# Optimization experiments

Measured on AMD Instinct MI355X. Metric: run time of the kernel, lower is better.

## Reference

```python
import jax, jax.numpy as jnp
import numpy as np

NUM_COND = 16  # num_conditions
EPS = 1e-5


def setup_inputs() -> dict:
    key = jax.random.key(0)
    k1, k2, k3, k4 = jax.random.split(key, 4)
    N, F = 500000, 128
    x = jax.random.normal(k1, (N, F), dtype=jnp.float32)
    labels = jax.random.randint(k2, (N,), 0, NUM_COND)
    gamma = jax.random.uniform(k3, (NUM_COND, F), dtype=jnp.float32)
    beta = jax.random.normal(k4, (NUM_COND, F), dtype=jnp.float32)
    return {"x": x, "labels": labels, "gamma": gamma, "beta": beta}


def reference(x, labels, gamma, beta):
    # Conditional BatchNorm1d (training mode): per-label batch statistics
    # over the samples of each group, then per-label affine transform.
    num_cond = gamma.shape[0]
    ones = jnp.ones((x.shape[0],), x.dtype)
    counts = jax.ops.segment_sum(ones, labels, num_segments=num_cond)   # [C]
    counts = jnp.maximum(counts, 1.0)                                    # guard empty groups
    s1 = jax.ops.segment_sum(x, labels, num_segments=num_cond)          # [C,F]
    s2 = jax.ops.segment_sum(x * x, labels, num_segments=num_cond)      # [C,F]
    mean = s1 / counts[:, None]
    var = s2 / counts[:, None] - mean * mean                             # biased var (BatchNorm)
    inv_std = jax.lax.rsqrt(var + EPS)                                   # [C,F]
    scale = gamma * inv_std                                              # [C,F]
    shift = beta - mean * scale                                          # [C,F]
    y = x * scale[labels] + shift[labels]                                # fused gather + affine
    return y
```

## Files before the change

kernel.cpp:

```cpp
#include <hip/hip_runtime.h>

#define NUM_COND 16
#define FDIM 128
#define EPS 1e-5f
#define WPB 2
#define NSLOT 3
#define PB 4160
#define NCHUNK 16
#define MAXNB 1024

typedef float __attribute__((ext_vector_type(4))) f4v;
__device__ __forceinline__ void nt_store4(float4* p, const float4& v) {
    f4v t = { v.x, v.y, v.z, v.w };
    __builtin_nontemporal_store(t, (f4v*)p);
}

__global__ __launch_bounds__(128) void cbn_stats_kernel(
    const float* __restrict__ x, const int* __restrict__ labels,
    float* __restrict__ ws, int N, int Npairs, int pchunk)
{
    __shared__ float acc[WPB][4096];
    __shared__ float stage[WPB][NSLOT * 256];
    const int t = threadIdx.x;
    const int w = t >> 6;
    const int lane = t & 63;
    const int half = lane >> 5;
    const int sl = lane & 31;

    {
        float4* z = (float4*)acc[w];
        for (int i = lane; i < 1024; i += 64) z[i] = make_float4(0.f, 0.f, 0.f, 0.f);
    }

    const int pbeg = blockIdx.x * pchunk;
    const int pend = min(Npairs, pbeg + pchunk);
    const float4* x4 = (const float4*)x;
    float2* r1 = (float2*)acc[w];
    float2* r2 = r1 + 1024;
    float4* stg4 = (float4*)stage[w];
    float2* stg2 = (float2*)stage[w];

    int cnt = 0;
    float4 v0, v1, v2;
    int la0 = 0, la1 = 0, la2 = 0, lb0 = 0, lb1 = 0, lb2 = 0;
    v0 = v1 = v2 = make_float4(0.f, 0.f, 0.f, 0.f);

#define LOADSLOT(S, P)                                                  \
    {   const int p_ = (P);                                             \
        if (p_ < pend) {                                                \
            const int r_ = min(2 * p_ + half, N - 1);                   \
            v##S = x4[(size_t)r_ * 32 + sl];                            \
            la##S = labels[2 * p_];                                     \
            lb##S = labels[min(2 * p_ + 1, N - 1)];                     \
        }                                                               \
    }

#define RMW(D, LB)                                                      \
    {   const int o_ = (LB) * 64 + lane;                                \
        float2 a_ = r1[o_];                                             \
        float2 b_ = r2[o_];                                             \
        a_.x += (D).x;                 a_.y += (D).y;                   \
        b_.x = fmaf((D).x, (D).x, b_.x);                                \
        b_.y = fmaf((D).y, (D).y, b_.y);                                \
        r1[o_] = a_;                                                    \
        r2[o_] = b_;                                                    \
        cnt += ((lane & 15) == (LB)) ? 1 : 0;                           \
    }

#define PROCSLOT(S, P)                                                  \
    {   const int p_ = (P);                                             \
        if (p_ < pend) {                                                \
            stg4[S * 64 + lane] = v##S;                                 \
            { float2 d_ = stg2[S * 128 + lane];        RMW(d_, la##S) } \
            if (2 * p_ + 1 < N) {                                       \
              float2 d_ = stg2[S * 128 + 64 + lane];   RMW(d_, lb##S) } \
        }                                                               \
    }

    int p = pbeg + w;
    LOADSLOT(0, p)
    LOADSLOT(1, p + WPB)
    LOADSLOT(2, p + 2 * WPB)

    for (; p < pend; p += NSLOT * WPB) {
        PROCSLOT(0, p)
        LOADSLOT(0, p + 3 * WPB)
        PROCSLOT(1, p + WPB)
        LOADSLOT(1, p + 4 * WPB)
        PROCSLOT(2, p + 2 * WPB)
        LOADSLOT(2, p + 5 * WPB)
    }

    __syncthreads();
    float* out = ws + (size_t)blockIdx.x * PB;
    for (int i = t; i < 4096; i += 128)
        out[i] = acc[0][i] + acc[1][i];
    if (lane < 16) out[4096 + w * 16 + lane] = (float)cnt;
}

__global__ __launch_bounds__(256) void cbn_reduce_kernel(
    const float* __restrict__ ws, float* __restrict__ ws2, int nb, int per)
{
    const int e = blockIdx.x * 256 + threadIdx.x;
    if (e >= PB) return;
    const int b0 = blockIdx.y * per;
    const int b1 = min(nb, b0 + per);
    float a = 0.f;
#pragma unroll 8
    for (int b = b0; b < b1; ++b) a += ws[(size_t)b * PB + e];
    ws2[(size_t)blockIdx.y * PB + e] = a;
}

__global__ __launch_bounds__(256) void cbn_finalize_kernel(
    const float* __restrict__ ws2, const float* __restrict__ gamma,
    const float* __restrict__ beta, float* __restrict__ scale_shift)
{
    const int e = blockIdx.x * 256 + threadIdx.x;
    const int lab = e >> 7;
    float a1 = 0.f, a2 = 0.f, cn = 0.f;
#pragma unroll
    for (int k = 0; k < NCHUNK; ++k) {
        const float* p = ws2 + (size_t)k * PB;
        a1 += p[e];
        a2 += p[2048 + e];
#pragma unroll
        for (int w2 = 0; w2 < WPB; ++w2)
            cn += p[4096 + w2 * 16 + lab];
    }
    cn = fmaxf(cn, 1.0f);
    const float mean = a1 / cn;
    const float var  = a2 / cn - mean * mean;
    const float sc = gamma[e] * rsqrtf(var + EPS);
    const float sh = beta[e] - mean * sc;
    scale_shift[e]        = sc;
    scale_shift[2048 + e] = sh;
}

__global__ __launch_bounds__(256) void cbn_apply_kernel(
    const float* __restrict__ x, const int* __restrict__ labels,
    const float* __restrict__ scale_shift, float* __restrict__ y, int N)
{
    __shared__ float4 ssc[NUM_COND * 32];
    __shared__ float4 ssh[NUM_COND * 32];
    const int t = threadIdx.x;
    const float4* ss4 = (const float4*)scale_shift;
    for (int i = t; i < NUM_COND * 32; i += 256) {
        ssc[i] = ss4[i];
        ssh[i] = ss4[512 + i];
    }
    __syncthreads();

    const int f4 = t & 31;
    const int rg = t >> 5;
    const float4* x4 = (const float4*)x;
    float4* y4 = (float4*)y;

    for (int base = blockIdx.x * 32 + rg; base < N; base += gridDim.x * 32) {
        const int r0 = base;
        int r1 = base + 8, r2 = base + 16, r3 = base + 24;
        const bool k1 = r1 < N, k2 = r2 < N, k3 = r3 < N;
        if (!k1) r1 = r0;  if (!k2) r2 = r0;  if (!k3) r3 = r0;

        const int l0 = labels[r0], l1 = labels[r1], l2 = labels[r2], l3 = labels[r3];
        const float4 v0 = x4[(size_t)r0 * 32 + f4];
        const float4 v1 = x4[(size_t)r1 * 32 + f4];
        const float4 v2 = x4[(size_t)r2 * 32 + f4];
        const float4 v3 = x4[(size_t)r3 * 32 + f4];

        const float4 c0 = ssc[l0 * 32 + f4], h0 = ssh[l0 * 32 + f4];
        const float4 c1 = ssc[l1 * 32 + f4], h1 = ssh[l1 * 32 + f4];
        const float4 c2 = ssc[l2 * 32 + f4], h2 = ssh[l2 * 32 + f4];
        const float4 c3 = ssc[l3 * 32 + f4], h3 = ssh[l3 * 32 + f4];

        float4 o0, o1, o2, o3;
        o0.x = fmaf(v0.x, c0.x, h0.x); o0.y = fmaf(v0.y, c0.y, h0.y);
        o0.z = fmaf(v0.z, c0.z, h0.z); o0.w = fmaf(v0.w, c0.w, h0.w);
        o1.x = fmaf(v1.x, c1.x, h1.x); o1.y = fmaf(v1.y, c1.y, h1.y);
        o1.z = fmaf(v1.z, c1.z, h1.z); o1.w = fmaf(v1.w, c1.w, h1.w);
        o2.x = fmaf(v2.x, c2.x, h2.x); o2.y = fmaf(v2.y, c2.y, h2.y);
        o2.z = fmaf(v2.z, c2.z, h2.z); o2.w = fmaf(v2.w, c2.w, h2.w);
        o3.x = fmaf(v3.x, c3.x, h3.x); o3.y = fmaf(v3.y, c3.y, h3.y);
        o3.z = fmaf(v3.z, c3.z, h3.z); o3.w = fmaf(v3.w, c3.w, h3.w);

        nt_store4(&y4[(size_t)r0 * 32 + f4], o0);
        if (k1) nt_store4(&y4[(size_t)r1 * 32 + f4], o1);
        if (k2) nt_store4(&y4[(size_t)r2 * 32 + f4], o2);
        if (k3) nt_store4(&y4[(size_t)r3 * 32 + f4], o3);
    }
}

extern "C" void kernel_launch(void* const* d_in, const int* in_sizes, int n_in,
                              void* d_out, int out_size, void* d_ws, size_t ws_size,
                              hipStream_t stream)
{
    const float* x      = (const float*)d_in[0];
    const int*   labels = (const int*)d_in[1];
    const float* gamma  = (const float*)d_in[2];
    const float* beta   = (const float*)d_in[3];
    float* y  = (float*)d_out;
    float* ws = (float*)d_ws;
    const int N = in_sizes[1];
    const int Npairs = (N + 1) / 2;

    const long floats = (long)(ws_size / sizeof(float));
    long avail = floats - (long)NCHUNK * PB - 4096;
    int nb = MAXNB;
    if ((long)nb * PB > avail) nb = (int)(avail / PB);
    if (nb < 1) nb = 1;
    const int pchunk = (Npairs + nb - 1) / nb;
    const int per    = (nb + NCHUNK - 1) / NCHUNK;

    float* ws2         = ws + (size_t)nb * PB;
    float* scale_shift = ws2 + (size_t)NCHUNK * PB;

    cbn_stats_kernel<<<nb, 128, 0, stream>>>(x, labels, ws, N, Npairs, pchunk);
    cbn_reduce_kernel<<<dim3((PB + 255) / 256, NCHUNK), 256, 0, stream>>>(ws, ws2, nb, per);
    cbn_finalize_kernel<<<8, 256, 0, stream>>>(ws2, gamma, beta, scale_shift);
    cbn_apply_kernel<<<2048, 256, 0, stream>>>(x, labels, scale_shift, y, N);
}
```

Before: 160.7 us.

## Drop LDS staging in stats kernel, accumulate float4 per half-wave, deepen prefetch

The stats kernel no longer stages loaded rows through shared memory and re-reads them as float2. Each half-wave now read-modify-writes float4 sums directly into its per-label accumulator. If both rows of a pair share a label, the two halves' updates run one after the other to avoid a race. Labels are loaded as int2 pairs, and counts are merged across halves with a shuffle. Blocks grow to 4 waves with 6 prefetch slots and half as many blocks, trading more LDS and registers for fewer LDS round trips and more loads in flight.

```diff
diff --git a/kernel.cpp b/kernel.cpp
--- a/kernel.cpp
+++ b/kernel.cpp
@@ -3,11 +3,11 @@
 #define NUM_COND 16
 #define FDIM 128
 #define EPS 1e-5f
-#define WPB 2
-#define NSLOT 3
+#define WPB 4
+#define NSLOT 6
 #define PB 4160
 #define NCHUNK 16
-#define MAXNB 1024
+#define MAXNB 512
 
 typedef float __attribute__((ext_vector_type(4))) f4v;
 __device__ __forceinline__ void nt_store4(float4* p, const float4& v) {
@@ -15,12 +15,11 @@
     __builtin_nontemporal_store(t, (f4v*)p);
 }
 
-__global__ __launch_bounds__(128) void cbn_stats_kernel(
+__global__ __launch_bounds__(256) void cbn_stats_kernel(
     const float* __restrict__ x, const int* __restrict__ labels,
     float* __restrict__ ws, int N, int Npairs, int pchunk)
 {
     __shared__ float acc[WPB][4096];
-    __shared__ float stage[WPB][NSLOT * 256];
     const int t = threadIdx.x;
     const int w = t >> 6;
     const int lane = t & 63;
@@ -35,45 +34,58 @@
     const int pbeg = blockIdx.x * pchunk;
     const int pend = min(Npairs, pbeg + pchunk);
     const float4* x4 = (const float4*)x;
-    float2* r1 = (float2*)acc[w];
-    float2* r2 = r1 + 1024;
-    float4* stg4 = (float4*)stage[w];
-    float2* stg2 = (float2*)stage[w];
+    const int2* lab2 = (const int2*)labels;
+    float4* r1 = (float4*)acc[w];
+    float4* r2 = r1 + 512;
 
     int cnt = 0;
-    float4 v0, v1, v2;
-    int la0 = 0, la1 = 0, la2 = 0, lb0 = 0, lb1 = 0, lb2 = 0;
-    v0 = v1 = v2 = make_float4(0.f, 0.f, 0.f, 0.f);
+    float4 v0, v1, v2, v3, v4, v5;
+    int la0 = 0, la1 = 0, la2 = 0, la3 = 0, la4 = 0, la5 = 0;
+    int lb0 = 0, lb1 = 0, lb2 = 0, lb3 = 0, lb4 = 0, lb5 = 0;
+    v0 = v1 = v2 = v3 = v4 = v5 = make_float4(0.f, 0.f, 0.f, 0.f);
 
 #define LOADSLOT(S, P)                                                  \
     {   const int p_ = (P);                                             \
         if (p_ < pend) {                                                \
             const int r_ = min(2 * p_ + half, N - 1);                   \
             v##S = x4[(size_t)r_ * 32 + sl];                            \
-            la##S = labels[2 * p_];                                     \
-            lb##S = labels[min(2 * p_ + 1, N - 1)];                     \
+            if (2 * p_ + 1 < N) {                                       \
+                const int2 L_ = lab2[p_];                               \
+                la##S = L_.x; lb##S = L_.y;                             \
+            } else {                                                    \
+                la##S = labels[2 * p_]; lb##S = la##S;                  \
+            }                                                           \
         }                                                               \
     }
 
-#define RMW(D, LB)                                                      \
-    {   const int o_ = (LB) * 64 + lane;                                \
-        float2 a_ = r1[o_];                                             \
-        float2 b_ = r2[o_];                                             \
-        a_.x += (D).x;                 a_.y += (D).y;                   \
-        b_.x = fmaf((D).x, (D).x, b_.x);                                \
-        b_.y = fmaf((D).y, (D).y, b_.y);                                \
+#define RMW4(LB, V)                                                     \
+    {   const int o_ = (LB) * 32 + sl;                                  \
+        float4 a_ = r1[o_];                                             \
+        float4 b_ = r2[o_];                                             \
+        a_.x += (V).x; a_.y += (V).y; a_.z += (V).z; a_.w += (V).w;     \
+        b_.x = fmaf((V).x, (V).x, b_.x);                                \
+        b_.y = fmaf((V).y, (V).y, b_.y);                                \
+        b_.z = fmaf((V).z, (V).z, b_.z);                                \
+        b_.w = fmaf((V).w, (V).w, b_.w);                                \
         r1[o_] = a_;                                                    \
         r2[o_] = b_;                                                    \
-        cnt += ((lane & 15) == (LB)) ? 1 : 0;                           \
     }
 
 #define PROCSLOT(S, P)                                                  \
     {   const int p_ = (P);                                             \
         if (p_ < pend) {                                                \
-            stg4[S * 64 + lane] = v##S;                                 \
-            { float2 d_ = stg2[S * 128 + lane];        RMW(d_, la##S) } \
-            if (2 * p_ + 1 < N) {                                       \
-              float2 d_ = stg2[S * 128 + 64 + lane];   RMW(d_, lb##S) } \
+            const bool odd_ok = (2 * p_ + 1 < N);                       \
+            const int sa_ = __builtin_amdgcn_readfirstlane(la##S);      \
+            const int sb_ = __builtin_amdgcn_readfirstlane(lb##S);      \
+            const int mylab = half ? lb##S : la##S;                     \
+            const bool act = (half == 0) || odd_ok;                     \
+            if (act) cnt += ((lane & 15) == mylab) ? 1 : 0;             \
+            if (sa_ != sb_) {                                           \
+                if (act) { RMW4(mylab, v##S) }                          \
+            } else {                                                    \
+                if (half == 0) { RMW4(la##S, v##S) }                    \
+                if (half == 1 && odd_ok) { RMW4(lb##S, v##S) }          \
+            }                                                           \
         }                                                               \
     }
 
@@ -81,21 +93,31 @@
     LOADSLOT(0, p)
     LOADSLOT(1, p + WPB)
     LOADSLOT(2, p + 2 * WPB)
+    LOADSLOT(3, p + 3 * WPB)
+    LOADSLOT(4, p + 4 * WPB)
+    LOADSLOT(5, p + 5 * WPB)
 
     for (; p < pend; p += NSLOT * WPB) {
         PROCSLOT(0, p)
-        LOADSLOT(0, p + 3 * WPB)
+        LOADSLOT(0, p + 6 * WPB)
         PROCSLOT(1, p + WPB)
-        LOADSLOT(1, p + 4 * WPB)
+        LOADSLOT(1, p + 7 * WPB)
         PROCSLOT(2, p + 2 * WPB)
-        LOADSLOT(2, p + 5 * WPB)
+        LOADSLOT(2, p + 8 * WPB)
+        PROCSLOT(3, p + 3 * WPB)
+        LOADSLOT(3, p + 9 * WPB)
+        PROCSLOT(4, p + 4 * WPB)
+        LOADSLOT(4, p + 10 * WPB)
+        PROCSLOT(5, p + 5 * WPB)
+        LOADSLOT(5, p + 11 * WPB)
     }
 
     __syncthreads();
     float* out = ws + (size_t)blockIdx.x * PB;
-    for (int i = t; i < 4096; i += 128)
-        out[i] = acc[0][i] + acc[1][i];
-    if (lane < 16) out[4096 + w * 16 + lane] = (float)cnt;
+    for (int i = t; i < 4096; i += 256)
+        out[i] = acc[0][i] + acc[1][i] + acc[2][i] + acc[3][i];
+    const int c2 = cnt + __shfl(cnt, lane ^ 32);
+    if (lane < 16) out[4096 + w * 16 + lane] = (float)c2;
 }
 
 __global__ __launch_bounds__(256) void cbn_reduce_kernel(
@@ -213,7 +235,7 @@
     float* ws2         = ws + (size_t)nb * PB;
     float* scale_shift = ws2 + (size_t)NCHUNK * PB;
 
-    cbn_stats_kernel<<<nb, 128, 0, stream>>>(x, labels, ws, N, Npairs, pchunk);
+    cbn_stats_kernel<<<nb, 256, 0, stream>>>(x, labels, ws, N, Npairs, pchunk);
     cbn_reduce_kernel<<<dim3((PB + 255) / 256, NCHUNK), 256, 0, stream>>>(ws, ws2, nb, per);
     cbn_finalize_kernel<<<8, 256, 0, stream>>>(ws2, gamma, beta, scale_shift);
     cbn_apply_kernel<<<2048, 256, 0, stream>>>(x, labels, scale_shift, y, N);
```

Result: no change. 162.9 us (+1.4%).
